# Kernel optimization log

Measured on AMD Instinct MI355X. Metric: run time of the kernel, lower is better.

The kernel has to match this reference:

```python
import jax, jax.numpy as jnp
import numpy as np

N = 100000   # nodes
E = 1600000  # edges
F = 64       # num_features
H = 64       # hidden_units
C = 10       # num_classes
G = 1000     # graphs in batch
BN_EPS = 1e-5


def setup_inputs() -> dict:
    key = jax.random.key(0)
    ks = jax.random.split(key, 32)
    inp = {
        "x": jax.random.normal(ks[0], (N, F), dtype=jnp.float32),
        "edge_index": jax.random.randint(ks[1], (2, E), 0, N, dtype=jnp.int64),
        "batch": jnp.sort(jax.random.randint(ks[2], (N,), 0, G, dtype=jnp.int64)),
    }
    i = 3
    def w(shape, scale):
        nonlocal i
        a = jax.random.normal(ks[i], shape, dtype=jnp.float32) * scale
        i += 1
        return a
    for l, din in [(0, F), (1, H)]:
        inp[f"c{l}_w1"] = w((din, H), 1.0 / np.sqrt(din))
        inp[f"c{l}_b1"] = jnp.zeros((H,), jnp.float32)
        inp[f"c{l}_g1"] = jnp.ones((H,), jnp.float32)
        inp[f"c{l}_be1"] = jnp.zeros((H,), jnp.float32)
        inp[f"c{l}_w2"] = w((H, H), 1.0 / np.sqrt(H))
        inp[f"c{l}_b2"] = jnp.zeros((H,), jnp.float32)
        inp[f"bn{l}_g"] = jnp.ones((H,), jnp.float32)
        inp[f"bn{l}_b"] = jnp.zeros((H,), jnp.float32)
    for l, din in [(0, F), (1, H), (2, H)]:
        inp[f"l{l}_w"] = w((din, C), 1.0 / np.sqrt(din))
        inp[f"l{l}_b"] = jnp.zeros((C,), jnp.float32)
    return inp


def _bn(h, g, b):
    # BatchNorm1d in training mode: batch statistics over node axis
    m = jnp.mean(h, axis=0)
    v = jnp.var(h, axis=0)
    return g * (h - m) * jax.lax.rsqrt(v + BN_EPS) + b


def _gin_conv(h, src, dst, w1, b1, g1, be1, w2, b2):
    # scatter-add neighbor aggregation: out[dst] += h[src]; eps = 0
    agg = jax.ops.segment_sum(h[src], dst, num_segments=N)
    z = h + agg                      # (1 + eps) * x + sum_j x_j
    z = jax.nn.relu(_bn(z @ w1 + b1, g1, be1))
    return z @ w2 + b2


def reference(x, edge_index, batch,
              c0_w1, c0_b1, c0_g1, c0_be1, c0_w2, c0_b2, bn0_g, bn0_b,
              c1_w1, c1_b1, c1_g1, c1_be1, c1_w2, c1_b2, bn1_g, bn1_b,
              l0_w, l0_b, l1_w, l1_b, l2_w, l2_b):
    src, dst = edge_index[0], edge_index[1]
    h0 = x
    h1 = jax.nn.relu(_bn(_gin_conv(h0, src, dst, c0_w1, c0_b1, c0_g1, c0_be1, c0_w2, c0_b2), bn0_g, bn0_b))
    h2 = jax.nn.relu(_bn(_gin_conv(h1, src, dst, c1_w1, c1_b1, c1_g1, c1_be1, c1_w2, c1_b2), bn1_g, bn1_b))
    # jumping-knowledge readout: per-layer global_add_pool -> Linear -> sum (dropout=0)
    out = jnp.zeros((G, C), dtype=x.dtype)
    for h, w, b in [(h0, l0_w, l0_b), (h1, l1_w, l1_b), (h2, l2_w, l2_b)]:
        pooled = jax.ops.segment_sum(h, batch, num_segments=G)
        out = out + pooled @ w + b
    return out
```

## Files before the change

kernel.cpp:

```cpp
#include <hip/hip_runtime.h>
#include <hip/hip_bf16.h>

#define BN_EPS 1e-5f
#define NBMAX 512
#define CHUNK 4096
#define CAP   5120
#define CAPC  6144

typedef __hip_bfloat16 bf16;
typedef __attribute__((ext_vector_type(8))) short short8;
typedef __attribute__((ext_vector_type(4))) float f32x4;

__device__ __forceinline__ float b2f(bf16 v) { return __bfloat162float(v); }
__device__ __forceinline__ bf16 f2b(float v) { return __float2bfloat16(v); }
__device__ __forceinline__ float bl(unsigned u) { return __uint_as_float(u << 16); }
__device__ __forceinline__ float bh(unsigned u) { return __uint_as_float(u & 0xffff0000u); }
__device__ __forceinline__ unsigned pack2(float x, float y) {
    union { bf16 b[2]; unsigned u; } p;
    p.b[0] = f2b(x); p.b[1] = f2b(y);
    return p.u;
}
__device__ __forceinline__ float bs2f(short s) {
    return __uint_as_float(((unsigned)(unsigned short)s) << 16);
}
__device__ __forceinline__ short f2bs(float v) {
    bf16 b = f2b(v);
    return *reinterpret_cast<short*>(&b);
}

__global__ __launch_bounds__(256) void initcast_k(
    const float* __restrict__ in, bf16* __restrict__ out, int total4,
    int* __restrict__ bcur, int NB)
{
    if (blockIdx.x == 0) {
        for (int i = threadIdx.x; i < NB; i += 256) bcur[i] = i * CAP;
    }
    int i = blockIdx.x * 256 + threadIdx.x;
    if (i >= total4) return;
    float4 v = ((const float4*)in)[i];
    union { ushort4 u; bf16 b[4]; } p;
    p.b[0] = f2b(v.x); p.b[1] = f2b(v.y); p.b[2] = f2b(v.z); p.b[3] = f2b(v.w);
    ((ushort4*)out)[i] = p.u;
}

__global__ __launch_bounds__(256) void binscatter_k(
    const int* __restrict__ src, const int* __restrict__ dst,
    int* __restrict__ bcur, int* __restrict__ tmp, int E, int NB)
{
    __shared__ int hist[NBMAX];
    __shared__ int loff[NBMAX];
    __shared__ int gb[NBMAX];
    __shared__ int lcur[NBMAX];
    __shared__ int staged[CHUNK];
    __shared__ unsigned short sb[CHUNK];
    __shared__ int ssc[256];
    const int t = threadIdx.x;
    for (int i = t; i < NB; i += 256) { hist[i] = 0; lcur[i] = 0; }
    __syncthreads();
    const int base = blockIdx.x * CHUNK;
    const int lim = min(CHUNK, E - base);
    int myb[16], myw[16];
    int cnt = 0;
    for (int i = t; i < lim; i += 256) {
        int d = dst[base + i];
        int s_ = src[base + i];
        int b = d >> 8;
        myb[cnt] = b;
        myw[cnt] = (s_ << 8) | (d & 255);
        cnt++;
        atomicAdd(&hist[b], 1);
    }
    __syncthreads();
    int v0 = (2 * t     < NB) ? hist[2 * t]     : 0;
    int v1 = (2 * t + 1 < NB) ? hist[2 * t + 1] : 0;
    ssc[t] = v0 + v1;
    __syncthreads();
    for (int off = 1; off < 256; off <<= 1) {
        int a = (t >= off) ? ssc[t - off] : 0;
        __syncthreads();
        ssc[t] += a;
        __syncthreads();
    }
    int excl = ssc[t] - (v0 + v1);
    if (2 * t < NB)     loff[2 * t] = excl;
    if (2 * t + 1 < NB) loff[2 * t + 1] = excl + v0;
    __syncthreads();
    for (int b = t; b < NB; b += 256)
        if (hist[b] > 0) gb[b] = atomicAdd(&bcur[b], hist[b]);
    for (int i = 0; i < cnt; i++) {
        int b = myb[i];
        int p = loff[b] + atomicAdd(&lcur[b], 1);
        staged[p] = myw[i];
        sb[p] = (unsigned short)b;
    }
    __syncthreads();
    for (int i = t; i < lim; i += 256) {
        int b = sb[i];
        tmp[gb[b] + (i - loff[b])] = staged[i];
    }
}

__global__ __launch_bounds__(256) void csr_k(
    const int* __restrict__ bcur, const int* __restrict__ tmp,
    int* __restrict__ rowptr, int* __restrict__ rowend,
    int* __restrict__ adj, int N)
{
    __shared__ int hist[256], pfx[256], cur[256], ssc[256];
    __shared__ int sadj[CAPC];
    const int b = blockIdx.x, t = threadIdx.x;
    const int lo = b * CAP;
    const int cnt = min(bcur[b] - lo, CAP);
    hist[t] = 0; cur[t] = 0;
    __syncthreads();
    for (int i = t; i < cnt; i += 256)
        atomicAdd(&hist[tmp[lo + i] & 255], 1);
    __syncthreads();
    int v = hist[t];
    ssc[t] = v;
    __syncthreads();
    for (int off = 1; off < 256; off <<= 1) {
        int a = (t >= off) ? ssc[t - off] : 0;
        __syncthreads();
        ssc[t] += a;
        __syncthreads();
    }
    pfx[t] = ssc[t] - v;
    const int node = b * 256 + t;
    if (node < N) {
        rowptr[node] = lo + pfx[t];
        rowend[node] = lo + pfx[t] + v;
    }
    __syncthreads();
    if (cnt <= CAPC) {
        for (int i = t; i < cnt; i += 256) {
            int w = tmp[lo + i];
            int d = w & 255;
            int p = pfx[d] + atomicAdd(&cur[d], 1);
            sadj[p] = w >> 8;
        }
        __syncthreads();
        for (int i = t; i < cnt; i += 256) adj[lo + i] = sadj[i];
    } else {
        for (int i = t; i < cnt; i += 256) {
            int w = tmp[lo + i];
            int d = w & 255;
            int p = pfx[d] + atomicAdd(&cur[d], 1);
            adj[lo + p] = w >> 8;
        }
    }
}

template<int AFFINE>
__global__ __launch_bounds__(256) void aggregate_k(
    const bf16* __restrict__ h, const int* __restrict__ rowptr,
    const int* __restrict__ rowend, const int* __restrict__ adj,
    bf16* __restrict__ z, int N,
    const float* __restrict__ sc, const float* __restrict__ sh)
{
    const int lane = threadIdx.x & 31;
    const int n = blockIdx.x * 8 + (threadIdx.x >> 5);
    float sc0 = 0.f, sc1 = 0.f, sh0 = 0.f, sh1 = 0.f;
    if (AFFINE) {
        const int f0 = lane * 2;
        sc0 = sc[f0]; sc1 = sc[f0 + 1];
        sh0 = sh[f0]; sh1 = sh[f0 + 1];
    }
    if (n >= N) return;
    const unsigned* hp = (const unsigned*)h;
    const int b = rowptr[n], e = rowend[n];

    unsigned u = hp[(size_t)n * 32 + lane];
    float a0 = bl(u), a1 = bh(u);
    if (AFFINE) {
        a0 = fmaxf(fmaf(a0, sc0, sh0), 0.f);
        a1 = fmaxf(fmaf(a1, sc1, sh1), 0.f);
    }
    float s0 = a0, s1 = a1;

    int i = b;
    for (; i + 16 <= e; i += 16) {
        int m[16];
        #pragma unroll
        for (int k = 0; k < 16; k++) m[k] = adj[i + k];
        unsigned w[16];
        #pragma unroll
        for (int k = 0; k < 16; k++) w[k] = hp[(size_t)m[k] * 32 + lane];
        #pragma unroll
        for (int k = 0; k < 16; k++) {
            float p0 = bl(w[k]), p1 = bh(w[k]);
            if (AFFINE) {
                p0 = fmaxf(fmaf(p0, sc0, sh0), 0.f);
                p1 = fmaxf(fmaf(p1, sc1, sh1), 0.f);
            }
            s0 += p0; s1 += p1;
        }
    }
    for (; i + 4 <= e; i += 4) {
        int m[4];
        #pragma unroll
        for (int k = 0; k < 4; k++) m[k] = adj[i + k];
        #pragma unroll
        for (int k = 0; k < 4; k++) {
            unsigned w = hp[(size_t)m[k] * 32 + lane];
            float p0 = bl(w), p1 = bh(w);
            if (AFFINE) {
                p0 = fmaxf(fmaf(p0, sc0, sh0), 0.f);
                p1 = fmaxf(fmaf(p1, sc1, sh1), 0.f);
            }
            s0 += p0; s1 += p1;
        }
    }
    for (; i < e; i++) {
        unsigned w = hp[(size_t)adj[i] * 32 + lane];
        float p0 = bl(w), p1 = bh(w);
        if (AFFINE) {
            p0 = fmaxf(fmaf(p0, sc0, sh0), 0.f);
            p1 = fmaxf(fmaf(p1, sc1, sh1), 0.f);
        }
        s0 += p0; s1 += p1;
    }
    ((unsigned*)z)[(size_t)n * 32 + lane] = pack2(s0, s1);
}

template<int MODE>
__global__ __launch_bounds__(256) void gemm64_k(
    const bf16* __restrict__ A,
    const float* __restrict__ scin, const float* __restrict__ shin,
    const float* __restrict__ W, const float* __restrict__ bias,
    bf16* __restrict__ out, float* __restrict__ pstat, int nrows)
{
    __shared__ bf16 sWt[64][72];
    __shared__ float sSc[64], sSh[64], sB[64];
    __shared__ float sredS[64][17], sredQ[64][17];
    const int tid = threadIdx.x;

    if (tid < 64) {
        sB[tid] = bias[tid];
        if (MODE == 1) { sSc[tid] = scin[tid]; sSh[tid] = shin[tid]; }
    }
    for (int i = tid; i < 4096; i += 256) {
        int k = i >> 6, n = i & 63;
        sWt[n][k] = f2b(W[i]);
    }
    __syncthreads();

    const int wave = tid >> 6, lane = tid & 63;
    const int quad = lane >> 4, l16 = lane & 15;
    const int row0 = blockIdx.x * 128 + wave * 32;

    short8 a[2][2];
    #pragma unroll
    for (int rt = 0; rt < 2; rt++) {
        int r = row0 + rt * 16 + l16;
        int rr = min(r, nrows - 1);
        const bf16* arow = A + (size_t)rr * 64;
        a[rt][0] = *(const short8*)(arow + quad * 8);
        a[rt][1] = *(const short8*)(arow + 32 + quad * 8);
        if (MODE == 1) {
            #pragma unroll
            for (int j = 0; j < 8; j++) {
                int f0 = quad * 8 + j;
                a[rt][0][j] = f2bs(fmaxf(fmaf(bs2f(a[rt][0][j]), sSc[f0], sSh[f0]), 0.f));
                int f1 = 32 + f0;
                a[rt][1][j] = f2bs(fmaxf(fmaf(bs2f(a[rt][1][j]), sSc[f1], sSh[f1]), 0.f));
            }
        }
    }

    float psS[4], psQ[4];
    #pragma unroll
    for (int t = 0; t < 4; t++) { psS[t] = 0.f; psQ[t] = 0.f; }

    #pragma unroll
    for (int t = 0; t < 4; t++) {
        const int n = t * 16 + l16;
        short8 b0 = *(const short8*)&sWt[n][quad * 8];
        short8 b1 = *(const short8*)&sWt[n][32 + quad * 8];
        const float bn_ = sB[n];
        #pragma unroll
        for (int rt = 0; rt < 2; rt++) {
            f32x4 acc = {0.f, 0.f, 0.f, 0.f};
            acc = __builtin_amdgcn_mfma_f32_16x16x32_bf16(a[rt][0], b0, acc, 0, 0, 0);
            acc = __builtin_amdgcn_mfma_f32_16x16x32_bf16(a[rt][1], b1, acc, 0, 0, 0);
            #pragma unroll
            for (int reg = 0; reg < 4; reg++) {
                int gr = row0 + rt * 16 + quad * 4 + reg;
                if (gr < nrows) {
                    float v = acc[reg] + bn_;
                    out[(size_t)gr * 64 + n] = f2b(v);
                    psS[t] += v;
                    psQ[t] = fmaf(v, v, psQ[t]);
                }
            }
        }
    }

    #pragma unroll
    for (int t = 0; t < 4; t++) {
        sredS[t * 16 + l16][wave * 4 + quad] = psS[t];
        sredQ[t * 16 + l16][wave * 4 + quad] = psQ[t];
    }
    __syncthreads();
    if (tid < 128) {
        const int c = tid & 63;
        const float* p = (tid < 64) ? &sredS[c][0] : &sredQ[c][0];
        float s = 0.f;
        #pragma unroll
        for (int i = 0; i < 16; i++) s += p[i];
        pstat[(size_t)blockIdx.x * 128 + (tid < 64 ? c : 64 + c)] = s;
    }
}

__global__ __launch_bounds__(256) void bn_reduce_k(
    const float* __restrict__ pstat, int nblk,
    const float* __restrict__ g, const float* __restrict__ be, float invN,
    float* __restrict__ sc, float* __restrict__ sh)
{
    const int f = blockIdx.x;
    const int t = threadIdx.x;
    float S = 0.f, Q = 0.f;
    for (int b = t; b < nblk; b += 256) {
        S += pstat[(size_t)b * 128 + f];
        Q += pstat[(size_t)b * 128 + 64 + f];
    }
    __shared__ float rs[256], rq[256];
    rs[t] = S; rq[t] = Q;
    __syncthreads();
    for (int off = 128; off > 0; off >>= 1) {
        if (t < off) { rs[t] += rs[t + off]; rq[t] += rq[t + off]; }
        __syncthreads();
    }
    if (t == 0) {
        float m = rs[0] * invN;
        float v = rq[0] * invN - m * m;
        float s = g[f] * rsqrtf(v + BN_EPS);
        sc[f] = s;
        sh[f] = be[f] - m * s;
    }
}

__global__ __launch_bounds__(256) void pool_readout_k(
    const bf16* __restrict__ xb, const bf16* __restrict__ z0,
    const bf16* __restrict__ z1, const int* __restrict__ batch,
    const float* __restrict__ scA, const float* __restrict__ shA,
    const float* __restrict__ scB, const float* __restrict__ shB,
    const float* __restrict__ w0, const float* __restrict__ b0,
    const float* __restrict__ w1, const float* __restrict__ b1,
    const float* __restrict__ w2, const float* __restrict__ b2,
    float* __restrict__ out, int Nn)
{
    const int g = blockIdx.x;
    int lo = 0, hi = Nn;
    while (lo < hi) { int mid = (lo + hi) >> 1; if (batch[mid] < g) lo = mid + 1; else hi = mid; }
    const int start = lo;
    hi = Nn;
    while (lo < hi) { int mid = (lo + hi) >> 1; if (batch[mid] <= g) lo = mid + 1; else hi = mid; }
    const int end = lo;

    const int f = threadIdx.x & 63;
    const int w = threadIdx.x >> 6;
    const float sA = scA[f], tA = shA[f];
    const float sB = scB[f], tB = shB[f];

    float s0 = 0.f, s1 = 0.f, s2 = 0.f;
    for (int i = start + w; i < end; i += 4) {
        s0 += b2f(xb[(size_t)i * 64 + f]);
        s1 += fmaxf(fmaf(b2f(z0[(size_t)i * 64 + f]), sA, tA), 0.f);
        s2 += fmaxf(fmaf(b2f(z1[(size_t)i * 64 + f]), sB, tB), 0.f);
    }
    __shared__ float p[3][4][64];
    p[0][w][f] = s0; p[1][w][f] = s1; p[2][w][f] = s2;
    __syncthreads();
    if (threadIdx.x < 10) {
        const int c = threadIdx.x;
        float acc = b0[c] + b1[c] + b2[c];
        for (int k = 0; k < 64; k++) {
            float q0 = p[0][0][k] + p[0][1][k] + p[0][2][k] + p[0][3][k];
            float q1 = p[1][0][k] + p[1][1][k] + p[1][2][k] + p[1][3][k];
            float q2 = p[2][0][k] + p[2][1][k] + p[2][2][k] + p[2][3][k];
            acc = fmaf(q0, w0[k * 10 + c], acc);
            acc = fmaf(q1, w1[k * 10 + c], acc);
            acc = fmaf(q2, w2[k * 10 + c], acc);
        }
        out[(size_t)g * 10 + c] = acc;
    }
}

extern "C" void kernel_launch(void* const* d_in, const int* in_sizes, int n_in,
                              void* d_out, int out_size, void* d_ws, size_t ws_size,
                              hipStream_t stream)
{
    const float* x     = (const float*)d_in[0];
    const int*   edge  = (const int*)d_in[1];
    const int*   batch = (const int*)d_in[2];
    const int N = in_sizes[0] / 64;
    const int E = in_sizes[1] / 2;
    const int G = out_size / 10;
    const int* src = edge;
    const int* dst = edge + E;
    const int NB = (N + 255) / 256;

    const float* c_w1[2]  = {(const float*)d_in[3],  (const float*)d_in[11]};
    const float* c_b1[2]  = {(const float*)d_in[4],  (const float*)d_in[12]};
    const float* c_g1[2]  = {(const float*)d_in[5],  (const float*)d_in[13]};
    const float* c_be1[2] = {(const float*)d_in[6],  (const float*)d_in[14]};
    const float* c_w2[2]  = {(const float*)d_in[7],  (const float*)d_in[15]};
    const float* c_b2[2]  = {(const float*)d_in[8],  (const float*)d_in[16]};
    const float* bn_g[2]  = {(const float*)d_in[9],  (const float*)d_in[17]};
    const float* bn_b[2]  = {(const float*)d_in[10], (const float*)d_in[18]};
    const float* lw[3]    = {(const float*)d_in[19], (const float*)d_in[21], (const float*)d_in[23]};
    const float* lb[3]    = {(const float*)d_in[20], (const float*)d_in[22], (const float*)d_in[24]};

    float* out = (float*)d_out;
    const size_t nh = (size_t)N * 64;
    const int PG = (N + 127) / 128;

    bf16*  zb    = (bf16*)d_ws;
    bf16*  wb    = zb + nh;
    bf16*  xb    = wb + nh;
    float* scsh  = (float*)(xb + nh);
    float* pstat = scsh + 512;
    int*   rowptr = (int*)(pstat + (size_t)PG * 128);
    int*   rowend = rowptr + N;
    int*   adj    = rowend + N;
    int*   tmp    = adj + (size_t)NB * CAP;
    int*   bcur   = tmp + (size_t)NB * CAP;

    float* sc0 = scsh;       float* sh0 = scsh + 64;
    float* scA = scsh + 128; float* shA = scsh + 192;
    float* sc2 = scsh + 256; float* sh2 = scsh + 320;
    float* scB = scsh + 384; float* shB = scsh + 448;

    const float invN = 1.0f / (float)N;
    const int binGrid  = (E + CHUNK - 1) / CHUNK;
    const int aggGrid  = (N + 7) / 8;
    const int ewGrid   = (int)((nh / 4 + 255) / 256);

    initcast_k<<<ewGrid, 256, 0, stream>>>(x, xb, (int)(nh / 4), bcur, NB);
    binscatter_k<<<binGrid, 256, 0, stream>>>(src, dst, bcur, tmp, E, NB);
    csr_k<<<NB, 256, 0, stream>>>(bcur, tmp, rowptr, rowend, adj, N);

    aggregate_k<0><<<aggGrid, 256, 0, stream>>>(xb, rowptr, rowend, adj, zb, N,
                                                nullptr, nullptr);
    gemm64_k<0><<<PG, 256, 0, stream>>>(zb, nullptr, nullptr,
                                        c_w1[0], c_b1[0], zb, pstat, N);
    bn_reduce_k<<<64, 256, 0, stream>>>(pstat, PG, c_g1[0], c_be1[0], invN, sc0, sh0);
    gemm64_k<1><<<PG, 256, 0, stream>>>(zb, sc0, sh0,
                                        c_w2[0], c_b2[0], zb, pstat, N);
    bn_reduce_k<<<64, 256, 0, stream>>>(pstat, PG, bn_g[0], bn_b[0], invN, scA, shA);

    aggregate_k<1><<<aggGrid, 256, 0, stream>>>(zb, rowptr, rowend, adj, wb, N,
                                                scA, shA);
    gemm64_k<0><<<PG, 256, 0, stream>>>(wb, nullptr, nullptr,
                                        c_w1[1], c_b1[1], wb, pstat, N);
    bn_reduce_k<<<64, 256, 0, stream>>>(pstat, PG, c_g1[1], c_be1[1], invN, sc2, sh2);
    gemm64_k<1><<<PG, 256, 0, stream>>>(wb, sc2, sh2,
                                        c_w2[1], c_b2[1], wb, pstat, N);
    bn_reduce_k<<<64, 256, 0, stream>>>(pstat, PG, bn_g[1], bn_b[1], invN, scB, shB);

    pool_readout_k<<<G, 256, 0, stream>>>(xb, zb, wb, batch,
                                          scA, shA, scB, shB,
                                          lw[0], lb[0], lw[1], lb[1], lw[2], lb[2],
                                          out, N);
}
```

Baseline: 309.9 us.

## Fuse BatchNorm stat reduction into GEMM tail via last-block ticket counter

Removes the four separate bn_reduce launches by having each GEMM block take an atomic ticket after writing its partial stats. The last 64 blocks to finish each spin until all blocks have arrived, then each reduces one feature's statistics and writes scale/shift. This saves kernel launch gaps and their serialization. In exchange it adds a spin-wait inside the kernel that depends on all blocks being resident or already finished, plus atomic and fence overhead, and it needs counters zeroed in initcast.

New measurement: 461.2 us. 1.49x slower.

```diff
diff --git a/kernel.cpp b/kernel.cpp
--- a/kernel.cpp
+++ b/kernel.cpp
@@ -30,10 +30,11 @@
 
 __global__ __launch_bounds__(256) void initcast_k(
     const float* __restrict__ in, bf16* __restrict__ out, int total4,
-    int* __restrict__ bcur, int NB)
+    int* __restrict__ bcur, int NB, unsigned* __restrict__ ctrs)
 {
     if (blockIdx.x == 0) {
         for (int i = threadIdx.x; i < NB; i += 256) bcur[i] = i * CAP;
+        if (threadIdx.x < 4) ctrs[threadIdx.x] = 0u;
     }
     int i = blockIdx.x * 256 + threadIdx.x;
     if (i >= total4) return;
@@ -227,11 +228,15 @@
     const bf16* __restrict__ A,
     const float* __restrict__ scin, const float* __restrict__ shin,
     const float* __restrict__ W, const float* __restrict__ bias,
-    bf16* __restrict__ out, float* __restrict__ pstat, int nrows)
+    bf16* __restrict__ out, float* __restrict__ pstat, int nrows,
+    unsigned* __restrict__ ctr, int PG,
+    const float* __restrict__ g, const float* __restrict__ be, float invN,
+    float* __restrict__ scout, float* __restrict__ shout)
 {
     __shared__ bf16 sWt[64][72];
     __shared__ float sSc[64], sSh[64], sB[64];
     __shared__ float sredS[64][17], sredQ[64][17];
+    __shared__ unsigned sTicket;
     const int tid = threadIdx.x;
 
     if (tid < 64) {
@@ -309,33 +314,41 @@
         for (int i = 0; i < 16; i++) s += p[i];
         pstat[(size_t)blockIdx.x * 128 + (tid < 64 ? c : 64 + c)] = s;
     }
-}
-
-__global__ __launch_bounds__(256) void bn_reduce_k(
-    const float* __restrict__ pstat, int nblk,
-    const float* __restrict__ g, const float* __restrict__ be, float invN,
-    float* __restrict__ sc, float* __restrict__ sh)
-{
-    const int f = blockIdx.x;
-    const int t = threadIdx.x;
-    float S = 0.f, Q = 0.f;
-    for (int b = t; b < nblk; b += 256) {
-        S += pstat[(size_t)b * 128 + f];
-        Q += pstat[(size_t)b * 128 + 64 + f];
-    }
-    __shared__ float rs[256], rq[256];
-    rs[t] = S; rq[t] = Q;
-    __syncthreads();
-    for (int off = 128; off > 0; off >>= 1) {
-        if (t < off) { rs[t] += rs[t + off]; rq[t] += rq[t + off]; }
-        __syncthreads();
-    }
-    if (t == 0) {
-        float m = rs[0] * invN;
-        float v = rq[0] * invN - m * m;
-        float s = g[f] * rsqrtf(v + BN_EPS);
-        sc[f] = s;
-        sh[f] = be[f] - m * s;
+
+    __syncthreads();
+    if (tid == 0) {
+        __threadfence();
+        sTicket = atomicAdd(ctr, 1u);
+    }
+    __syncthreads();
+    const int ticket = (int)sTicket;
+    if (ticket >= PG - 64) {
+        if (tid == 0) {
+            while (atomicAdd(ctr, 0u) < (unsigned)PG) __builtin_amdgcn_s_sleep(2);
+        }
+        __syncthreads();
+        __threadfence();
+        const int f = ticket - (PG - 64);
+        float S = 0.f, Q = 0.f;
+        for (int b = tid; b < PG; b += 256) {
+            S += pstat[(size_t)b * 128 + f];
+            Q += pstat[(size_t)b * 128 + 64 + f];
+        }
+        float* rs = &sredS[0][0];
+        float* rq = &sredQ[0][0];
+        rs[tid] = S; rq[tid] = Q;
+        __syncthreads();
+        for (int off = 128; off > 0; off >>= 1) {
+            if (tid < off) { rs[tid] += rs[tid + off]; rq[tid] += rq[tid + off]; }
+            __syncthreads();
+        }
+        if (tid == 0) {
+            float m = rs[0] * invN;
+            float v = rq[0] * invN - m * m;
+            float s = g[f] * rsqrtf(v + BN_EPS);
+            scout[f] = s;
+            shout[f] = be[f] - m * s;
+        }
     }
 }
 
@@ -425,6 +438,7 @@
     int*   adj    = rowend + N;
     int*   tmp    = adj + (size_t)NB * CAP;
     int*   bcur   = tmp + (size_t)NB * CAP;
+    unsigned* ctrs = (unsigned*)(bcur + NB);
 
     float* sc0 = scsh;       float* sh0 = scsh + 64;
     float* scA = scsh + 128; float* shA = scsh + 192;
@@ -436,27 +450,27 @@
     const int aggGrid  = (N + 7) / 8;
     const int ewGrid   = (int)((nh / 4 + 255) / 256);
 
-    initcast_k<<<ewGrid, 256, 0, stream>>>(x, xb, (int)(nh / 4), bcur, NB);
+    initcast_k<<<ewGrid, 256, 0, stream>>>(x, xb, (int)(nh / 4), bcur, NB, ctrs);
     binscatter_k<<<binGrid, 256, 0, stream>>>(src, dst, bcur, tmp, E, NB);
     csr_k<<<NB, 256, 0, stream>>>(bcur, tmp, rowptr, rowend, adj, N);
 
     aggregate_k<0><<<aggGrid, 256, 0, stream>>>(xb, rowptr, rowend, adj, zb, N,
                                                 nullptr, nullptr);
     gemm64_k<0><<<PG, 256, 0, stream>>>(zb, nullptr, nullptr,
-                                        c_w1[0], c_b1[0], zb, pstat, N);
-    bn_reduce_k<<<64, 256, 0, stream>>>(pstat, PG, c_g1[0], c_be1[0], invN, sc0, sh0);
+                                        c_w1[0], c_b1[0], zb, pstat, N,
+                                        ctrs + 0, PG, c_g1[0], c_be1[0], invN, sc0, sh0);
     gemm64_k<1><<<PG, 256, 0, stream>>>(zb, sc0, sh0,
-                                        c_w2[0], c_b2[0], zb, pstat, N);
-    bn_reduce_k<<<64, 256, 0, stream>>>(pstat, PG, bn_g[0], bn_b[0], invN, scA, shA);
+                                        c_w2[0], c_b2[0], zb, pstat, N,
+                                        ctrs + 1, PG, bn_g[0], bn_b[0], invN, scA, shA);
 
     aggregate_k<1><<<aggGrid, 256, 0, stream>>>(zb, rowptr, rowend, adj, wb, N,
                                                 scA, shA);
     gemm64_k<0><<<PG, 256, 0, stream>>>(wb, nullptr, nullptr,
-                                        c_w1[1], c_b1[1], wb, pstat, N);
-    bn_reduce_k<<<64, 256, 0, stream>>>(pstat, PG, c_g1[1], c_be1[1], invN, sc2, sh2);
+                                        c_w1[1], c_b1[1], wb, pstat, N,
+                                        ctrs + 2, PG, c_g1[1], c_be1[1], invN, sc2, sh2);
     gemm64_k<1><<<PG, 256, 0, stream>>>(wb, sc2, sh2,
-                                        c_w2[1], c_b2[1], wb, pstat, N);
-    bn_reduce_k<<<64, 256, 0, stream>>>(pstat, PG, bn_g[1], bn_b[1], invN, scB, shB);
+                                        c_w2[1], c_b2[1], wb, pstat, N,
+                                        ctrs + 3, PG, bn_g[1], bn_b[1], invN, scB, shB);
 
     pool_readout_k<<<G, 256, 0, stream>>>(xb, zb, wb, batch,
                                           scA, shA, scB, shB,
```
